# Optimization experiments

Measured on AMD Instinct MI355X. Metric: run time of the kernel, lower is better.

Reference implementation:

```python
import jax, jax.numpy as jnp
import numpy as np

N = 100000   # nodes
E = 1600000  # edges
B = 128      # graphs
VOCAB, EMB, HID = 10000, 128, 128


def gcn_conv(x, src, dst, ew, W, b, n_nodes):
    # PyG GCNConv: x' = D^{-1/2}(A_w + I) D^{-1/2} (x W) + b, self-loop weight 1
    x = x @ W  # [N, H]
    loop = jnp.arange(n_nodes)
    src2 = jnp.concatenate([src, loop])
    dst2 = jnp.concatenate([dst, loop])
    ew2 = jnp.concatenate([ew, jnp.ones((n_nodes,), x.dtype)])
    deg = jax.ops.segment_sum(ew2, dst2, num_segments=n_nodes)
    dinv = jnp.where(deg > 0, deg ** -0.5, 0.0)
    norm = dinv[src2] * ew2 * dinv[dst2]                      # [E+N]
    msg = x[src2] * norm[:, None]                             # gather-scale
    out = jax.ops.segment_sum(msg, dst2, num_segments=n_nodes)  # scatter-add
    return out + b


def setup_inputs() -> dict:
    key = jax.random.key(0)
    ks = jax.random.split(key, 12)
    x_idx = jax.random.randint(ks[0], (N,), 0, VOCAB)
    edge_index = jax.random.randint(ks[1], (2, E), 0, N)
    edge_weight = jax.random.uniform(ks[2], (E,), jnp.float32)
    batch = jnp.sort(jax.random.randint(ks[3], (N,), 0, B))
    emb_table = jax.random.normal(ks[4], (VOCAB, EMB), jnp.float32)
    emb_table = emb_table.at[0].set(0.0)  # padding_idx=0
    s = 1.0 / np.sqrt(EMB)
    W1 = jax.random.uniform(ks[5], (EMB, HID), jnp.float32, -s, s)
    b1 = jnp.zeros((HID,), jnp.float32)
    W2 = jax.random.uniform(ks[6], (HID, HID), jnp.float32, -s, s)
    b2 = jnp.zeros((HID,), jnp.float32)
    mlp_W1 = jax.random.uniform(ks[7], (HID, HID // 2), jnp.float32, -s, s)
    mlp_b1 = jax.random.uniform(ks[8], (HID // 2,), jnp.float32, -s, s)
    s2 = 1.0 / np.sqrt(HID // 2)
    mlp_W2 = jax.random.uniform(ks[9], (HID // 2, 2), jnp.float32, -s2, s2)
    mlp_b2 = jax.random.uniform(ks[10], (2,), jnp.float32, -s2, s2)
    return dict(x_idx=x_idx, edge_index=edge_index, edge_weight=edge_weight,
                batch=batch, emb_table=emb_table, W1=W1, b1=b1, W2=W2, b2=b2,
                mlp_W1=mlp_W1, mlp_b1=mlp_b1, mlp_W2=mlp_W2, mlp_b2=mlp_b2)


def reference(x_idx, edge_index, edge_weight, batch, emb_table, W1, b1, W2, b2,
              mlp_W1, mlp_b1, mlp_W2, mlp_b2):
    src, dst = edge_index[0], edge_index[1]
    x = emb_table[x_idx]                                  # embedding lookup
    x = jax.nn.relu(gcn_conv(x, src, dst, edge_weight, W1, b1, N))
    # dropout is inference no-op
    x = jax.nn.relu(gcn_conv(x, src, dst, edge_weight, W2, b2, N))
    # global mean pool over graphs
    sums = jax.ops.segment_sum(x, batch, num_segments=B)
    cnts = jax.ops.segment_sum(jnp.ones((N,), x.dtype), batch, num_segments=B)
    g = sums / jnp.maximum(cnts, 1.0)[:, None]            # [B, HID]
    h = jax.nn.relu(g @ mlp_W1 + mlp_b1)
    out = h @ mlp_W2 + mlp_b2
    return jax.nn.softmax(out, axis=1)
```

## Files before the change

kernel.cpp:

```cpp
#include <hip/hip_runtime.h>
#include <hip/hip_bf16.h>

#define NN 100000
#define NE 1600000
#define NB 128
#define NV 10000
#define HD 128

#define NBUCK 782
#define EBLK 512
#define EPB (NE / EBLK)

using bf16x8 = __attribute__((ext_vector_type(8))) short;
using f32x4  = __attribute__((ext_vector_type(4))) float;
typedef __attribute__((ext_vector_type(8))) unsigned short ushortv8;
typedef __attribute__((ext_vector_type(8))) unsigned char ucharv8;
typedef float f32x2 __attribute__((ext_vector_type(2)));

__device__ __forceinline__ float bf2f(unsigned short b) {
  return __uint_as_float((unsigned)b << 16);
}
__device__ __forceinline__ unsigned short f2bf(float f) {
  __hip_bfloat16 h = __float2bfloat16(f);
  return *reinterpret_cast<unsigned short*>(&h);
}
__device__ __forceinline__ unsigned char f2fp8(float f) {
  return (unsigned char)(__builtin_amdgcn_cvt_pk_fp8_f32(f, 0.f, 0, false) & 0xff);
}
__device__ __forceinline__ unsigned packSN(unsigned s, float v) {
  return (s << 15) | ((unsigned)f2bf(v) & 0x7fffu);
}
__device__ __forceinline__ float unpackN(unsigned u) {
  return __uint_as_float((u & 0x7fffu) << 16);
}
__device__ __forceinline__ void acc16(float* acc, uint4 u, float c) {
  f32x2 v;
  v = __builtin_amdgcn_cvt_pk_f32_fp8((int)u.x, false); acc[0] += c*v[0]; acc[1] += c*v[1];
  v = __builtin_amdgcn_cvt_pk_f32_fp8((int)u.x, true);  acc[2] += c*v[0]; acc[3] += c*v[1];
  v = __builtin_amdgcn_cvt_pk_f32_fp8((int)u.y, false); acc[4] += c*v[0]; acc[5] += c*v[1];
  v = __builtin_amdgcn_cvt_pk_f32_fp8((int)u.y, true);  acc[6] += c*v[0]; acc[7] += c*v[1];
  v = __builtin_amdgcn_cvt_pk_f32_fp8((int)u.z, false); acc[8] += c*v[0]; acc[9] += c*v[1];
  v = __builtin_amdgcn_cvt_pk_f32_fp8((int)u.z, true);  acc[10]+= c*v[0]; acc[11]+= c*v[1];
  v = __builtin_amdgcn_cvt_pk_f32_fp8((int)u.w, false); acc[12]+= c*v[0]; acc[13]+= c*v[1];
  v = __builtin_amdgcn_cvt_pk_f32_fp8((int)u.w, true);  acc[14]+= c*v[0]; acc[15]+= c*v[1];
}


__global__ __launch_bounds__(1024) void k_bcount(const int* __restrict__ dst,
                                                 int* __restrict__ cntmat) {
  __shared__ int h[NBUCK];
  int t = threadIdx.x, blk = blockIdx.x;
  for (int i = t; i < NBUCK; i += 1024) h[i] = 0;
  __syncthreads();
  int base = blk * EPB;
  for (int i = t; i < EPB; i += 1024) atomicAdd(&h[dst[base + i] >> 7], 1);
  __syncthreads();
  for (int i = t; i < NBUCK; i += 1024) cntmat[(size_t)blk * NBUCK + i] = h[i];
}

__global__ __launch_bounds__(256) void k_cscan(int* __restrict__ cntmat,
                                               int* __restrict__ totals) {
  __shared__ int sh[256];
  int bu = blockIdx.x, t = threadIdx.x;
  int v0 = cntmat[(size_t)(2 * t) * NBUCK + bu];
  int v1 = cntmat[(size_t)(2 * t + 1) * NBUCK + bu];
  int s = v0 + v1;
  sh[t] = s;
  __syncthreads();
  #pragma unroll
  for (int off = 1; off < 256; off <<= 1) {
    int u = (t >= off) ? sh[t - off] : 0;
    __syncthreads();
    sh[t] += u;
    __syncthreads();
  }
  int pre = sh[t] - s;
  cntmat[(size_t)(2 * t) * NBUCK + bu] = pre;
  cntmat[(size_t)(2 * t + 1) * NBUCK + bu] = pre + v0;
  if (t == 255) totals[bu] = sh[255];
}

__global__ __launch_bounds__(1024) void k_tscan(const int* __restrict__ totals,
                                                int* __restrict__ bucketBase) {
  __shared__ int sh[1024];
  int t = threadIdx.x;
  int v = (t < NBUCK) ? totals[t] : 0;
  sh[t] = v;
  __syncthreads();
  #pragma unroll
  for (int off = 1; off < 1024; off <<= 1) {
    int u = (t >= off) ? sh[t - off] : 0;
    __syncthreads();
    sh[t] += u;
    __syncthreads();
  }
  if (t < NBUCK) bucketBase[t] = sh[t] - v;
  if (t == NBUCK - 1) bucketBase[NBUCK] = sh[t];
}

__global__ __launch_bounds__(1024) void k_bscatter(const int* __restrict__ src,
                                                   const int* __restrict__ dst,
                                                   const float* __restrict__ ew,
                                                   const int* __restrict__ cntmat,
                                                   const int* __restrict__ bucketBase,
                                                   uint2* __restrict__ spair) {
  __shared__ int off[NBUCK];
  int t = threadIdx.x, blk = blockIdx.x;
  for (int i = t; i < NBUCK; i += 1024)
    off[i] = bucketBase[i] + cntmat[(size_t)blk * NBUCK + i];
  __syncthreads();
  int base = blk * EPB;
  for (int i = t; i < EPB; i += 1024) {
    int e = base + i;
    int d = dst[e];
    unsigned pew = packSN((unsigned)src[e], ew[e]);
    int pos = atomicAdd(&off[d >> 7], 1);
    spair[pos] = make_uint2(pew, (unsigned)(d & 127));
  }
}

__global__ __launch_bounds__(256) void k_bdeg(const uint2* __restrict__ spair,
                                              const int* __restrict__ bucketBase,
                                              int* __restrict__ rowptr,
                                              float* __restrict__ dinv) {
  __shared__ int cnt[128];
  __shared__ float ws[128];
  __shared__ int sh[128];
  int bu = blockIdx.x, t = threadIdx.x;
  if (t < 128) { cnt[t] = 0; ws[t] = 0.f; }
  __syncthreads();
  int ebeg = bucketBase[bu], eend = bucketBase[bu + 1];
  for (int e = ebeg + t; e < eend; e += 256) {
    uint2 p = spair[e];
    atomicAdd(&cnt[p.y], 1);
    atomicAdd(&ws[p.y], unpackN(p.x));
  }
  __syncthreads();
  int v = 0;
  if (t < 128) { v = cnt[t]; sh[t] = v; }
  __syncthreads();
  #pragma unroll
  for (int off = 1; off < 128; off <<= 1) {
    int u = 0;
    if (t < 128 && t >= off) u = sh[t - off];
    __syncthreads();
    if (t < 128) sh[t] += u;
    __syncthreads();
  }
  if (t < 128) {
    int gid = (bu << 7) + t;
    if (gid < NN) {
      rowptr[gid] = ebeg + sh[t] - v;
      dinv[gid] = rsqrtf(1.0f + ws[t]);
    }
    if (gid == NN) rowptr[NN] = NE;
  }
}

__global__ __launch_bounds__(256) void k_bfill(const uint2* __restrict__ spair,
                                               const int* __restrict__ bucketBase,
                                               const int* __restrict__ rowptr,
                                               const float* __restrict__ dinv,
                                               unsigned* __restrict__ csr) {
  __shared__ int cnt[128];
  __shared__ float sdv[128];
  __shared__ int srp[128];
  int bu = blockIdx.x, t = threadIdx.x;
  if (t < 128) {
    cnt[t] = 0;
    int gid = (bu << 7) + t;
    if (gid < NN) { sdv[t] = dinv[gid]; srp[t] = rowptr[gid]; }
  }
  __syncthreads();
  int ebeg = bucketBase[bu], eend = bucketBase[bu + 1];
  for (int e = ebeg + t; e < eend; e += 256) {
    uint2 p = spair[e];
    int dl = (int)p.y;
    unsigned s = p.x >> 15;
    float ewf = unpackN(p.x);
    int r = atomicAdd(&cnt[dl], 1);
    float nrm = dinv[s] * ewf * sdv[dl];
    csr[srp[dl] + r] = packSN(s, nrm);
  }
}

__global__ void k_trans(const unsigned* __restrict__ csrS,
                        const int* __restrict__ xidx,
                        unsigned* __restrict__ csrV) {
  int i = blockIdx.x * blockDim.x + threadIdx.x;
  if (i < NE) {
    unsigned u = csrS[i];
    csrV[i] = ((unsigned)xidx[u >> 15] << 15) | (u & 0x7fffu);
  }
}

__global__ void k_wprep2(const float* __restrict__ W1, const float* __restrict__ W2,
                         unsigned short* __restrict__ Wt1, unsigned short* __restrict__ Wt2) {
  int t = blockIdx.x * blockDim.x + threadIdx.x;
  const float* W = (t < 16384) ? W1 : W2;
  unsigned short* Wt = (t < 16384) ? Wt1 : Wt2;
  int i = t & 16383;
  int k = i >> 7, n = i & 127;
  Wt[n * 128 + k] = f2bf(W[k * 128 + n]);
}

template <bool AF32>
__global__ __launch_bounds__(256) void k_gemm_mfma(const void* __restrict__ Av,
                                                   const unsigned short* __restrict__ Wt,
                                                   unsigned char* __restrict__ C, int M) {
  __shared__ unsigned char Cs[128][132];
  const int t = threadIdx.x;
  const int wave = t >> 6, lane = t & 63;
  const int lrow = lane & 15, lk = lane >> 4;
  const int row0 = blockIdx.x * 128;
  const int wrow = row0 + wave * 32;

  f32x4 acc[2][8];
  #pragma unroll
  for (int i = 0; i < 2; ++i)
    #pragma unroll
    for (int j = 0; j < 8; ++j) acc[i][j] = (f32x4){0.f, 0.f, 0.f, 0.f};

  #pragma unroll
  for (int kt = 0; kt < 4; ++kt) {
    bf16x8 a[2];
    #pragma unroll
    for (int rt = 0; rt < 2; ++rt) {
      int r = wrow + rt * 16 + lrow;
      bf16x8 av = (bf16x8){0, 0, 0, 0, 0, 0, 0, 0};
      if (r < M) {
        if (AF32) {
          const float* ap = (const float*)Av + (size_t)r * HD + kt * 32 + lk * 8;
          #pragma unroll
          for (int j = 0; j < 8; ++j) av[j] = (short)f2bf(ap[j]);
        } else {
          av = *(const bf16x8*)((const unsigned short*)Av + (size_t)r * HD + kt * 32 + lk * 8);
        }
      }
      a[rt] = av;
    }
    #pragma unroll
    for (int ct = 0; ct < 8; ++ct) {
      bf16x8 b = *(const bf16x8*)(Wt + (size_t)(ct * 16 + lrow) * HD + kt * 32 + lk * 8);
      acc[0][ct] = __builtin_amdgcn_mfma_f32_16x16x32_bf16(a[0], b, acc[0][ct], 0, 0, 0);
      acc[1][ct] = __builtin_amdgcn_mfma_f32_16x16x32_bf16(a[1], b, acc[1][ct], 0, 0, 0);
    }
  }

  #pragma unroll
  for (int rt = 0; rt < 2; ++rt)
    #pragma unroll
    for (int ct = 0; ct < 8; ++ct)
      #pragma unroll
      for (int reg = 0; reg < 4; ++reg) {
        int lr = wave * 32 + rt * 16 + lk * 4 + reg;
        Cs[lr][ct * 16 + lrow] = f2fp8(acc[rt][ct][reg]);
      }
  __syncthreads();

  #pragma unroll
  for (int i = 0; i < 8; ++i) {
    int idx = t + i * 256;
    int r = idx >> 4;
    int c = (idx & 15) * 8;
    int gr = row0 + r;
    if (gr < M)
      *(ucharv8*)(C + (size_t)gr * HD + c) = *(const ucharv8*)&Cs[r][c];
  }
}

template <bool SELFIND, bool POOL>
__global__ __launch_bounds__(256) void k_agg8(const unsigned char* __restrict__ xw,
                                              const int* __restrict__ xidx,
                                              const int* __restrict__ rowptr,
                                              const unsigned* __restrict__ csr,
                                              const float* __restrict__ dinv,
                                              const float* __restrict__ bias,
                                              unsigned short* __restrict__ outp,
                                              const int* __restrict__ batch,
                                              float* __restrict__ sums) {
  int t = threadIdx.x;
  int n = blockIdx.x * 32 + (t >> 3);
  int lane = t & 7;
  int beg = rowptr[n], end = rowptr[n + 1];

  int sn = SELFIND ? xidx[n] : n;
  uint4 uself = *(const uint4*)(xw + (size_t)sn * HD + lane * 16);

  float acc[16];
  #pragma unroll
  for (int j = 0; j < 16; ++j) acc[j] = 0.f;

  auto quad = [&](uint4 q) {
    int s0 = (int)(q.x >> 15), s1 = (int)(q.y >> 15);
    int s2 = (int)(q.z >> 15), s3 = (int)(q.w >> 15);
    uint4 u0 = *(const uint4*)(xw + (size_t)s0 * HD + lane * 16);
    uint4 u1 = *(const uint4*)(xw + (size_t)s1 * HD + lane * 16);
    uint4 u2 = *(const uint4*)(xw + (size_t)s2 * HD + lane * 16);
    uint4 u3 = *(const uint4*)(xw + (size_t)s3 * HD + lane * 16);
    acc16(acc, u0, unpackN(q.x)); acc16(acc, u1, unpackN(q.y));
    acc16(acc, u2, unpackN(q.z)); acc16(acc, u3, unpackN(q.w));
  };

  int e = beg;
  int alignEnd = min(end, (beg + 3) & ~3);
  for (; e < alignEnd; ++e) {
    unsigned u = csr[e];
    int s0 = (int)(u >> 15);
    float c0 = unpackN(u);
    uint4 u0 = *(const uint4*)(xw + (size_t)s0 * HD + lane * 16);
    acc16(acc, u0, c0);
  }
  int nquad = (end - e) >> 2;
  if (nquad > 0) {
    uint4 q = *(const uint4*)(csr + e);
    for (int i = 1; i < nquad; ++i) {
      uint4 qn = *(const uint4*)(csr + e + 4 * i);
      quad(q);
      q = qn;
    }
    quad(q);
    e += nquad * 4;
  }
  for (; e < end; ++e) {
    unsigned u = csr[e];
    int s0 = (int)(u >> 15);
    float c0 = unpackN(u);
    uint4 u0 = *(const uint4*)(xw + (size_t)s0 * HD + lane * 16);
    acc16(acc, u0, c0);
  }

  float d = dinv[n];
  acc16(acc, uself, d * d);

  const float4* bp = reinterpret_cast<const float4*>(bias + lane * 16);
  float4 b0 = bp[0], b1 = bp[1], b2 = bp[2], b3 = bp[3];
  float o[16];
  o[0]  = fmaxf(acc[0]  + b0.x, 0.f); o[1]  = fmaxf(acc[1]  + b0.y, 0.f);
  o[2]  = fmaxf(acc[2]  + b0.z, 0.f); o[3]  = fmaxf(acc[3]  + b0.w, 0.f);
  o[4]  = fmaxf(acc[4]  + b1.x, 0.f); o[5]  = fmaxf(acc[5]  + b1.y, 0.f);
  o[6]  = fmaxf(acc[6]  + b1.z, 0.f); o[7]  = fmaxf(acc[7]  + b1.w, 0.f);
  o[8]  = fmaxf(acc[8]  + b2.x, 0.f); o[9]  = fmaxf(acc[9]  + b2.y, 0.f);
  o[10] = fmaxf(acc[10] + b2.z, 0.f); o[11] = fmaxf(acc[11] + b2.w, 0.f);
  o[12] = fmaxf(acc[12] + b3.x, 0.f); o[13] = fmaxf(acc[13] + b3.y, 0.f);
  o[14] = fmaxf(acc[14] + b3.z, 0.f); o[15] = fmaxf(acc[15] + b3.w, 0.f);

  if constexpr (!POOL) {
    ushortv8 r0, r1;
    #pragma unroll
    for (int j = 0; j < 8; ++j) { r0[j] = f2bf(o[j]); r1[j] = f2bf(o[8 + j]); }
    *(ushortv8*)(outp + (size_t)n * HD + lane * 16) = r0;
    *(ushortv8*)(outp + (size_t)n * HD + lane * 16 + 8) = r1;
  } else {
    __shared__ float pool[32][129];
    __shared__ int ib[32];
    int nl = t >> 3;
    #pragma unroll
    for (int j = 0; j < 16; ++j) pool[nl][lane * 16 + j] = o[j];
    if (t < 32) ib[t] = batch[blockIdx.x * 32 + t];
    __syncthreads();
    if (t < 128) {
      float a = 0.f;
      int c = t;
      #pragma unroll 4
      for (int i = 0; i < 32; ++i) {
        a += pool[i][c];
        if (i == 31 || ib[i + 1] != ib[i]) {
          atomicAdd(&sums[(size_t)ib[i] * HD + c], a);
          a = 0.f;
        }
      }
    }
  }
}

__global__ __launch_bounds__(256) void k_zero_counts(float* __restrict__ sums,
                                                     const int* __restrict__ batch,
                                                     float* __restrict__ cnt) {
  int i = blockIdx.x * blockDim.x + threadIdx.x;
  if (i < NB * HD) sums[i] = 0.f;
  if (blockIdx.x == 0 && threadIdx.x < NB) {
    int b = threadIdx.x;
    auto lb = [&](int v) {
      int lo = 0, hi = NN;
      while (lo < hi) { int m = (lo + hi) >> 1; if (batch[m] < v) lo = m + 1; else hi = m; }
      return lo;
    };
    cnt[b] = (float)(lb(b + 1) - lb(b));
  }
}

__global__ __launch_bounds__(64) void k_head(const float* __restrict__ sums,
                                             const float* __restrict__ cnt,
                                             const float* __restrict__ W1,
                                             const float* __restrict__ b1,
                                             const float* __restrict__ W2,
                                             const float* __restrict__ b2,
                                             float* __restrict__ out) {
  int g = blockIdx.x, t = threadIdx.x;
  __shared__ float gv[128];
  __shared__ float h[64];
  __shared__ float logits[2];
  float c = fmaxf(cnt[g], 1.0f);
  gv[t] = sums[g * HD + t] / c;
  gv[t + 64] = sums[g * HD + 64 + t] / c;
  __syncthreads();
  float acc = b1[t];
  for (int k = 0; k < 128; ++k) acc += gv[k] * W1[k * 64 + t];
  h[t] = fmaxf(acc, 0.f);
  __syncthreads();
  if (t < 2) {
    float a = b2[t];
    for (int j = 0; j < 64; ++j) a += h[j] * W2[j * 2 + t];
    logits[t] = a;
  }
  __syncthreads();
  if (t < 2) {
    float m = fmaxf(logits[0], logits[1]);
    float e0 = __expf(logits[0] - m), e1 = __expf(logits[1] - m);
    out[g * 2 + t] = (t == 0 ? e0 : e1) / (e0 + e1);
  }
}

extern "C" void kernel_launch(void* const* d_in, const int* in_sizes, int n_in,
                              void* d_out, int out_size, void* d_ws, size_t ws_size,
                              hipStream_t stream) {
  const int*   x_idx = (const int*)d_in[0];
  const int*   eidx  = (const int*)d_in[1];
  const float* ew    = (const float*)d_in[2];
  const int*   batch = (const int*)d_in[3];
  const float* emb   = (const float*)d_in[4];
  const float* W1    = (const float*)d_in[5];
  const float* b1    = (const float*)d_in[6];
  const float* W2    = (const float*)d_in[7];
  const float* b2    = (const float*)d_in[8];
  const float* mW1   = (const float*)d_in[9];
  const float* mb1   = (const float*)d_in[10];
  const float* mW2   = (const float*)d_in[11];
  const float* mb2   = (const float*)d_in[12];
  const int* src = eidx;
  const int* dst = eidx + NE;
  float* out = (float*)d_out;

  char* ws = (char*)d_ws;
  size_t off = 0;
  auto alloc = [&](size_t bytes) {
    void* p = ws + off;
    off += (bytes + 255) & ~(size_t)255;
    return p;
  };
  int*   cntmat     = (int*)alloc((size_t)EBLK * NBUCK * 4);
  int*   totals     = (int*)alloc((size_t)NBUCK * 4);
  int*   bucketBase = (int*)alloc((size_t)(NBUCK + 1) * 4);
  int*   rowptr     = (int*)alloc((size_t)(NN + 1) * 4);
  float* dinv       = (float*)alloc((size_t)NN * 4);
  unsigned* csrS    = (unsigned*)alloc((size_t)NE * 4);
  unsigned* csrV    = (unsigned*)alloc((size_t)NE * 4);
  unsigned short* Wt1  = (unsigned short*)alloc((size_t)HD * HD * 2);
  unsigned short* Wt2  = (unsigned short*)alloc((size_t)HD * HD * 2);
  unsigned char* embW  = (unsigned char*)alloc((size_t)NV * HD);
  unsigned char* bufA  = (unsigned char*)alloc((size_t)NN * HD);
  float* sums    = (float*)alloc((size_t)NB * HD * 4);
  float* cnt     = (float*)alloc((size_t)NB * 4);
  char* unionReg = (char*)alloc((size_t)NN * HD * 2);
  uint2* spair = (uint2*)unionReg;
  unsigned short* bufB = (unsigned short*)unionReg;

  k_bcount<<<EBLK, 1024, 0, stream>>>(dst, cntmat);
  k_cscan<<<NBUCK, 256, 0, stream>>>(cntmat, totals);
  k_tscan<<<1, 1024, 0, stream>>>(totals, bucketBase);
  k_bscatter<<<EBLK, 1024, 0, stream>>>(src, dst, ew, cntmat, bucketBase, spair);
  k_bdeg<<<NBUCK, 256, 0, stream>>>(spair, bucketBase, rowptr, dinv);
  k_bfill<<<NBUCK, 256, 0, stream>>>(spair, bucketBase, rowptr, dinv, csrS);
  k_trans<<<(NE + 255) / 256, 256, 0, stream>>>(csrS, x_idx, csrV);

  k_wprep2<<<128, 256, 0, stream>>>(W1, W2, Wt1, Wt2);

  k_gemm_mfma<true><<<(NV + 127) / 128, 256, 0, stream>>>(emb, Wt1, embW, NV);

  k_zero_counts<<<64, 256, 0, stream>>>(sums, batch, cnt);

  k_agg8<true, false><<<NN / 32, 256, 0, stream>>>(
      embW, x_idx, rowptr, csrV, dinv, b1, bufB, nullptr, nullptr);

  k_gemm_mfma<false><<<(NN + 127) / 128, 256, 0, stream>>>(bufB, Wt2, bufA, NN);
  k_agg8<false, true><<<NN / 32, 256, 0, stream>>>(
      bufA, nullptr, rowptr, csrS, dinv, b2, nullptr, batch, sums);

  k_head<<<NB, 64, 0, stream>>>(sums, cnt, mW1, mb1, mW2, mb2, out);
}
```

Before: 194.1 us.

## Fuse degree and fill kernels, fold source dinv into GEMM epilogue

Merges k_bdeg and k_bfill into one kernel, so spair is read twice within one launch and rowptr/dinv stay in shared memory instead of going through global memory. The per-edge dinv[src] gather is removed from the fill. For layer 2, the src-side dinv scaling moves into the second GEMM epilogue, which scales each row by dinv and adjusts the self-loop weight to match. Layer 1 applies dinv[src] inside k_trans. The zero/count kernel is folded into k_tscan, which saves a launch but adds serial work to a single-block kernel, and the fp8 rounding of the dinv-scaled values changes slightly.

```diff
diff --git a/kernel.cpp b/kernel.cpp
--- a/kernel.cpp
+++ b/kernel.cpp
@@ -81,7 +81,10 @@
 }
 
 __global__ __launch_bounds__(1024) void k_tscan(const int* __restrict__ totals,
-                                                int* __restrict__ bucketBase) {
+                                                int* __restrict__ bucketBase,
+                                                float* __restrict__ sums,
+                                                const int* __restrict__ batch,
+                                                float* __restrict__ cnt) {
   __shared__ int sh[1024];
   int t = threadIdx.x;
   int v = (t < NBUCK) ? totals[t] : 0;
@@ -96,6 +99,16 @@
   }
   if (t < NBUCK) bucketBase[t] = sh[t] - v;
   if (t == NBUCK - 1) bucketBase[NBUCK] = sh[t];
+  #pragma unroll
+  for (int i = 0; i < 16; ++i) sums[t + i * 1024] = 0.f;
+  if (t < NB) {
+    auto lb = [&](int x) {
+      int lo = 0, hi = NN;
+      while (lo < hi) { int m = (lo + hi) >> 1; if (batch[m] < x) lo = m + 1; else hi = m; }
+      return lo;
+    };
+    cnt[t] = (float)(lb(t + 1) - lb(t));
+  }
 }
 
 __global__ __launch_bounds__(1024) void k_bscatter(const int* __restrict__ src,
@@ -119,13 +132,16 @@
   }
 }
 
-__global__ __launch_bounds__(256) void k_bdeg(const uint2* __restrict__ spair,
-                                              const int* __restrict__ bucketBase,
-                                              int* __restrict__ rowptr,
-                                              float* __restrict__ dinv) {
+__global__ __launch_bounds__(256) void k_bdegfill(const uint2* __restrict__ spair,
+                                                  const int* __restrict__ bucketBase,
+                                                  int* __restrict__ rowptr,
+                                                  float* __restrict__ dinv,
+                                                  unsigned* __restrict__ csr) {
   __shared__ int cnt[128];
   __shared__ float ws[128];
   __shared__ int sh[128];
+  __shared__ float sdv[128];
+  __shared__ int srp[128];
   int bu = blockIdx.x, t = threadIdx.x;
   if (t < 128) { cnt[t] = 0; ws[t] = 0.f; }
   __syncthreads();
@@ -149,48 +165,34 @@
   }
   if (t < 128) {
     int gid = (bu << 7) + t;
-    if (gid < NN) {
-      rowptr[gid] = ebeg + sh[t] - v;
-      dinv[gid] = rsqrtf(1.0f + ws[t]);
-    }
+    int rp = ebeg + sh[t] - v;
+    float dv = rsqrtf(1.0f + ws[t]);
+    srp[t] = rp;
+    sdv[t] = dv;
+    if (gid < NN) { rowptr[gid] = rp; dinv[gid] = dv; }
     if (gid == NN) rowptr[NN] = NE;
-  }
-}
-
-__global__ __launch_bounds__(256) void k_bfill(const uint2* __restrict__ spair,
-                                               const int* __restrict__ bucketBase,
-                                               const int* __restrict__ rowptr,
-                                               const float* __restrict__ dinv,
-                                               unsigned* __restrict__ csr) {
-  __shared__ int cnt[128];
-  __shared__ float sdv[128];
-  __shared__ int srp[128];
-  int bu = blockIdx.x, t = threadIdx.x;
-  if (t < 128) {
     cnt[t] = 0;
-    int gid = (bu << 7) + t;
-    if (gid < NN) { sdv[t] = dinv[gid]; srp[t] = rowptr[gid]; }
-  }
-  __syncthreads();
-  int ebeg = bucketBase[bu], eend = bucketBase[bu + 1];
+  }
+  __syncthreads();
   for (int e = ebeg + t; e < eend; e += 256) {
     uint2 p = spair[e];
     int dl = (int)p.y;
-    unsigned s = p.x >> 15;
-    float ewf = unpackN(p.x);
     int r = atomicAdd(&cnt[dl], 1);
-    float nrm = dinv[s] * ewf * sdv[dl];
-    csr[srp[dl] + r] = packSN(s, nrm);
+    float nrm = unpackN(p.x) * sdv[dl];
+    csr[srp[dl] + r] = packSN(p.x >> 15, nrm);
   }
 }
 
 __global__ void k_trans(const unsigned* __restrict__ csrS,
                         const int* __restrict__ xidx,
+                        const float* __restrict__ dinv,
                         unsigned* __restrict__ csrV) {
   int i = blockIdx.x * blockDim.x + threadIdx.x;
   if (i < NE) {
     unsigned u = csrS[i];
-    csrV[i] = ((unsigned)xidx[u >> 15] << 15) | (u & 0x7fffu);
+    unsigned s = u >> 15;
+    float nrm = unpackN(u) * dinv[s];
+    csrV[i] = packSN((unsigned)xidx[s], nrm);
   }
 }
 
@@ -204,16 +206,23 @@
   Wt[n * 128 + k] = f2bf(W[k * 128 + n]);
 }
 
-template <bool AF32>
+template <bool AF32, bool SCALE>
 __global__ __launch_bounds__(256) void k_gemm_mfma(const void* __restrict__ Av,
                                                    const unsigned short* __restrict__ Wt,
-                                                   unsigned char* __restrict__ C, int M) {
+                                                   unsigned char* __restrict__ C, int M,
+                                                   const float* __restrict__ dv) {
   __shared__ unsigned char Cs[128][132];
+  __shared__ float sdvv[128];
   const int t = threadIdx.x;
   const int wave = t >> 6, lane = t & 63;
   const int lrow = lane & 15, lk = lane >> 4;
   const int row0 = blockIdx.x * 128;
   const int wrow = row0 + wave * 32;
+
+  if (SCALE) {
+    if (t < 128) sdvv[t] = (row0 + t < M) ? dv[row0 + t] : 1.f;
+    __syncthreads();
+  }
 
   f32x4 acc[2][8];
   #pragma unroll
@@ -254,7 +263,9 @@
       #pragma unroll
       for (int reg = 0; reg < 4; ++reg) {
         int lr = wave * 32 + rt * 16 + lk * 4 + reg;
-        Cs[lr][ct * 16 + lrow] = f2fp8(acc[rt][ct][reg]);
+        float x = acc[rt][ct][reg];
+        if (SCALE) x *= sdvv[lr];
+        Cs[lr][ct * 16 + lrow] = f2fp8(x);
       }
   __syncthreads();
 
@@ -269,7 +280,7 @@
   }
 }
 
-template <bool SELFIND, bool POOL>
+template <bool SELFIND, bool SCALED, bool POOL>
 __global__ __launch_bounds__(256) void k_agg8(const unsigned char* __restrict__ xw,
                                               const int* __restrict__ xidx,
                                               const int* __restrict__ rowptr,
@@ -331,7 +342,7 @@
   }
 
   float d = dinv[n];
-  acc16(acc, uself, d * d);
+  acc16(acc, uself, SCALED ? d : d * d);
 
   const float4* bp = reinterpret_cast<const float4*>(bias + lane * 16);
   float4 b0 = bp[0], b1 = bp[1], b2 = bp[2], b3 = bp[3];
@@ -371,22 +382,6 @@
         }
       }
     }
-  }
-}
-
-__global__ __launch_bounds__(256) void k_zero_counts(float* __restrict__ sums,
-                                                     const int* __restrict__ batch,
-                                                     float* __restrict__ cnt) {
-  int i = blockIdx.x * blockDim.x + threadIdx.x;
-  if (i < NB * HD) sums[i] = 0.f;
-  if (blockIdx.x == 0 && threadIdx.x < NB) {
-    int b = threadIdx.x;
-    auto lb = [&](int v) {
-      int lo = 0, hi = NN;
-      while (lo < hi) { int m = (lo + hi) >> 1; if (batch[m] < v) lo = m + 1; else hi = m; }
-      return lo;
-    };
-    cnt[b] = (float)(lb(b + 1) - lb(b));
   }
 }
 
@@ -468,23 +463,22 @@
 
   k_bcount<<<EBLK, 1024, 0, stream>>>(dst, cntmat);
   k_cscan<<<NBUCK, 256, 0, stream>>>(cntmat, totals);
-  k_tscan<<<1, 1024, 0, stream>>>(totals, bucketBase);
+  k_tscan<<<1, 1024, 0, stream>>>(totals, bucketBase, sums, batch, cnt);
   k_bscatter<<<EBLK, 1024, 0, stream>>>(src, dst, ew, cntmat, bucketBase, spair);
-  k_bdeg<<<NBUCK, 256, 0, stream>>>(spair, bucketBase, rowptr, dinv);
-  k_bfill<<<NBUCK, 256, 0, stream>>>(spair, bucketBase, rowptr, dinv, csrS);
-  k_trans<<<(NE + 255) / 256, 256, 0, stream>>>(csrS, x_idx, csrV);
+  k_bdegfill<<<NBUCK, 256, 0, stream>>>(spair, bucketBase, rowptr, dinv, csrS);
+  k_trans<<<(NE + 255) / 256, 256, 0, stream>>>(csrS, x_idx, dinv, csrV);
 
   k_wprep2<<<128, 256, 0, stream>>>(W1, W2, Wt1, Wt2);
 
-  k_gemm_mfma<true><<<(NV + 127) / 128, 256, 0, stream>>>(emb, Wt1, embW, NV);
-
-  k_zero_counts<<<64, 256, 0, stream>>>(sums, batch, cnt);
-
-  k_agg8<true, false><<<NN / 32, 256, 0, stream>>>(
+  k_gemm_mfma<true, false><<<(NV + 127) / 128, 256, 0, stream>>>(
+      emb, Wt1, embW, NV, nullptr);
+
+  k_agg8<true, false, false><<<NN / 32, 256, 0, stream>>>(
       embW, x_idx, rowptr, csrV, dinv, b1, bufB, nullptr, nullptr);
 
-  k_gemm_mfma<false><<<(NN + 127) / 128, 256, 0, stream>>>(bufB, Wt2, bufA, NN);
-  k_agg8<false, true><<<NN / 32, 256, 0, stream>>>(
+  k_gemm_mfma<false, true><<<(NN + 127) / 128, 256, 0, stream>>>(
+      bufB, Wt2, bufA, NN, dinv);
+  k_agg8<false, true, true><<<NN / 32, 256, 0, stream>>>(
       bufA, nullptr, rowptr, csrS, dinv, b2, nullptr, batch, sums);
 
   k_head<<<NB, 64, 0, stream>>>(sums, cnt, mW1, mb1, mW2, mb2, out);
```

Measured after the change: 189.9 us. 2.2% less time.
